# Kernel tuning notes

Measured on AMD Instinct MI355X. Metric: run time of the kernel, lower is better.

## Reference

```python
import jax, jax.numpy as jnp
import numpy as np

B, L, D, C, NB = 2, 256, 3, 256, 64
LN_EPS = 1e-5


def setup_inputs() -> dict:
    ks = jax.random.split(jax.random.key(0), 12)
    x_BLD = jax.random.normal(ks[0], (B, L, D), dtype=jnp.float32) * 0.5
    c_BD = jax.random.normal(ks[1], (B, C), dtype=jnp.float32)
    embed_w = jax.random.normal(ks[2], (NB, C), dtype=jnp.float32) * 0.02
    pos_w = jax.random.normal(ks[3], (128, C), dtype=jnp.float32) * 0.02
    bins = jnp.linspace(0.0, 3.0, NB - 1, dtype=jnp.float32)
    ada_w = jax.random.normal(ks[4], (3 * C, C), dtype=jnp.float32) * (C ** -0.5)
    ada_b = jnp.zeros((3 * C,), dtype=jnp.float32)
    ln_g = jnp.ones((C,), dtype=jnp.float32)
    ln_b = jnp.zeros((C,), dtype=jnp.float32)
    fc1_w = jax.random.normal(ks[5], (4 * C, C), dtype=jnp.float32) * (C ** -0.5)
    fc1_b = jnp.zeros((4 * C,), dtype=jnp.float32)
    fc2_w = jax.random.normal(ks[6], (C, 4 * C), dtype=jnp.float32) * ((4 * C) ** -0.5)
    fc2_b = jnp.zeros((C,), dtype=jnp.float32)
    return {"x_BLD": x_BLD, "c_BD": c_BD, "embed_w": embed_w, "pos_w": pos_w,
            "bins": bins, "ada_w": ada_w, "ada_b": ada_b, "ln_g": ln_g,
            "ln_b": ln_b, "fc1_w": fc1_w, "fc1_b": fc1_b, "fc2_w": fc2_w,
            "fc2_b": fc2_b}


def reference(x_BLD, c_BD, embed_w, pos_w, bins, ada_w, ada_b, ln_g, ln_b,
              fc1_w, fc1_b, fc2_w, fc2_b):
    # pairwise squared distances: [B, L, L]
    d_BLL = jnp.sum((x_BLD[:, :, None, :] - x_BLD[:, None, :, :]) ** 2, axis=-1)
    # bucketize (torch.bucketize right=False == searchsorted side='left')
    idx_BLL = jnp.searchsorted(bins, d_BLL, side="left")
    # relative position embedding: [L, L, C]
    rel = jnp.arange(L)[:, None] - jnp.arange(L)[None, :]
    rel = jnp.clip(rel, -64, 63) + 64
    pos_LLD = pos_w[rel]
    # adaLN modulation from conditioning: SiLU -> Linear -> 3 chunks
    mod = jax.nn.silu(c_BD) @ ada_w.T + ada_b            # [B, 3C]
    shift, scale, gate = jnp.split(mod, 3, axis=-1)      # each [B, C]
    shift = shift[:, None, None, :]
    scale = scale[:, None, None, :]
    gate = gate[:, None, None, :]
    # embed + pos, affine modulate
    s = embed_w[idx_BLL] + pos_LLD[None]                 # [B, L, L, C]
    s = s * (1.0 + scale) + shift
    # LayerNorm over channel dim
    mu = jnp.mean(s, axis=-1, keepdims=True)
    var = jnp.mean((s - mu) ** 2, axis=-1, keepdims=True)
    h = (s - mu) * jax.lax.rsqrt(var + LN_EPS) * ln_g + ln_b
    # MLP: Linear -> GELU(exact) -> Linear
    h = jax.nn.gelu(h @ fc1_w.T + fc1_b, approximate=False)
    h = h @ fc2_w.T + fc2_b
    return s + gate * h
```

## Files before the change

kernel.cpp:

```cpp
#include <hip/hip_runtime.h>
#include <math.h>

#define Cn 256
#define Ln 256
#define Bn 2
#define H1 1024
#define NIDX 64
#define NREL 128
#define NCOMBO 16384
#define BK 64
#define TROWS 32

typedef __attribute__((ext_vector_type(8))) short bf16x8;
typedef __attribute__((ext_vector_type(4))) float f32x4;
typedef unsigned int u32;

__device__ __forceinline__ float gelu_exact(float x) {
    return 0.5f * x * (1.0f + erff(x * 0.70710678118654752f));
}
__device__ __forceinline__ short f2bf(float f) {
    unsigned u = __float_as_uint(f);
    return (short)((u + 0x7fffu + ((u >> 16) & 1u)) >> 16);
}
__device__ __forceinline__ void async16(const void* g, void* l) {
    __builtin_amdgcn_global_load_lds((const __attribute__((address_space(1))) u32*)g,
                                     (__attribute__((address_space(3))) u32*)l, 16, 0, 0);
}

__global__ __launch_bounds__(256) void mod_kernel(
    const float* __restrict__ c_BD, const float* __restrict__ ada_w,
    const float* __restrict__ ada_b, float* __restrict__ mod)
{
    int o = blockIdx.x * 256 + threadIdx.x;
    int b = o / (3 * Cn);
    int j = o - b * (3 * Cn);
    const float* crow = c_BD + b * Cn;
    const float* wrow = ada_w + (size_t)j * Cn;
    float acc = 0.f;
    for (int k = 0; k < Cn; k += 4) {
        float4 cv = *(const float4*)(crow + k);
        float4 wv = *(const float4*)(wrow + k);
        acc += (cv.x / (1.f + expf(-cv.x))) * wv.x;
        acc += (cv.y / (1.f + expf(-cv.y))) * wv.y;
        acc += (cv.z / (1.f + expf(-cv.z))) * wv.z;
        acc += (cv.w / (1.f + expf(-cv.w))) * wv.w;
    }
    mod[o] = acc + ada_b[j];
}

__global__ __launch_bounds__(256) void cvt_kernel(
    const float* __restrict__ s, short* __restrict__ d, int n)
{
    int i = (blockIdx.x * 256 + threadIdx.x) * 4;
    if (i < n) {
        float4 v = *(const float4*)(s + i);
        short4 o;
        o.x = f2bf(v.x); o.y = f2bf(v.y); o.z = f2bf(v.z); o.w = f2bf(v.w);
        *(short4*)(d + i) = o;
    }
}

__global__ __launch_bounds__(256) void ln_kernel(
    const float* __restrict__ embed_w, const float* __restrict__ pos_w,
    const float* __restrict__ ln_g, const float* __restrict__ ln_b,
    const float* __restrict__ mod,
    float* __restrict__ s_out, short* __restrict__ h_out)
{
    const int tid  = threadIdx.x;
    const int wave = tid >> 6;
    const int lane = tid & 63;
    const int base = blockIdx.x * 8;
    const int b    = base >> 13;
    const int idx  = (base >> 7) & 63;
    const int rel0 = base & 127;
    const float* modb = mod + b * (3 * Cn);
    const int c0 = lane * 4;

    const float4 ev = *(const float4*)(embed_w + (size_t)idx * Cn + c0);
    const float4 sc = *(const float4*)(modb + Cn + c0);
    const float4 sh = *(const float4*)(modb + c0);
    const float4 lg = *(const float4*)(ln_g + c0);
    const float4 lb = *(const float4*)(ln_b + c0);

    #pragma unroll
    for (int r8 = 0; r8 < 2; ++r8) {
        const int rr  = wave * 2 + r8;
        const int row = base + rr;
        const float4 p = *(const float4*)(pos_w + (size_t)(rel0 + rr) * Cn + c0);
        float v0 = (ev.x + p.x) * (1.f + sc.x) + sh.x;
        float v1 = (ev.y + p.y) * (1.f + sc.y) + sh.y;
        float v2 = (ev.z + p.z) * (1.f + sc.z) + sh.z;
        float v3 = (ev.w + p.w) * (1.f + sc.w) + sh.w;
        float sum = v0 + v1 + v2 + v3;
        #pragma unroll
        for (int off = 32; off; off >>= 1) sum += __shfl_xor(sum, off, 64);
        const float mu = sum * (1.f / Cn);
        float t0 = v0 - mu, t1 = v1 - mu, t2 = v2 - mu, t3 = v3 - mu;
        float p2 = t0 * t0 + t1 * t1 + t2 * t2 + t3 * t3;
        #pragma unroll
        for (int off = 32; off; off >>= 1) p2 += __shfl_xor(p2, off, 64);
        const float rstd = rsqrtf(p2 * (1.f / Cn) + 1e-5f);

        *(float4*)(s_out + (size_t)row * Cn + c0) = (float4){v0, v1, v2, v3};
        short4 hq;
        hq.x = f2bf(t0 * rstd * lg.x + lb.x);
        hq.y = f2bf(t1 * rstd * lg.y + lb.y);
        hq.z = f2bf(t2 * rstd * lg.z + lb.z);
        hq.w = f2bf(t3 * rstd * lg.w + lb.w);
        *(short4*)(h_out + (size_t)row * Cn + c0) = hq;
    }
}

__global__ __launch_bounds__(256) void gemm1_kernel(
    const short* __restrict__ h, const short* __restrict__ w1,
    const float* __restrict__ fc1_b, short* __restrict__ g)
{
    __shared__ __align__(16) short Alds[128 * BK];
    __shared__ __align__(16) short Wlds[128 * BK];

    const int tid  = threadIdx.x;
    const int wave = tid >> 6;
    const int lane = tid & 63;
    const int quad = lane >> 4;
    const int l15  = lane & 15;
    const int wm   = wave >> 1, wn = wave & 1;
    const int m0 = (blockIdx.x >> 3) * 128;
    const int n0 = (blockIdx.x & 7) * 128;

    const int srow = lane >> 3;
    const int skel = (lane & 7) * 8;

    f32x4 acc[4][4];
    #pragma unroll
    for (int a = 0; a < 4; ++a)
        #pragma unroll
        for (int c = 0; c < 4; ++c) acc[a][c] = (f32x4){0.f, 0.f, 0.f, 0.f};

    for (int kt = 0; kt < Cn; kt += BK) {
        #pragma unroll
        for (int c = 0; c < 4; ++c) {
            const int r = wave * 32 + c * 8;
            async16(h  + (size_t)(m0 + r + srow) * Cn + kt + skel, Alds + r * BK);
            async16(w1 + (size_t)(n0 + r + srow) * Cn + kt + skel, Wlds + r * BK);
        }
        __syncthreads();
        #pragma unroll
        for (int ks = 0; ks < 2; ++ks) {
            bf16x8 wf[4], hf[4];
            #pragma unroll
            for (int nt = 0; nt < 4; ++nt)
                wf[nt] = *(const bf16x8*)(Wlds + (wn * 64 + nt * 16 + l15) * BK + ks * 32 + quad * 8);
            #pragma unroll
            for (int mt = 0; mt < 4; ++mt)
                hf[mt] = *(const bf16x8*)(Alds + (wm * 64 + mt * 16 + l15) * BK + ks * 32 + quad * 8);
            #pragma unroll
            for (int mt = 0; mt < 4; ++mt)
                #pragma unroll
                for (int nt = 0; nt < 4; ++nt)
                    acc[mt][nt] = __builtin_amdgcn_mfma_f32_16x16x32_bf16(
                        wf[nt], hf[mt], acc[mt][nt], 0, 0, 0);
        }
        __syncthreads();
    }

    #pragma unroll
    for (int mt = 0; mt < 4; ++mt) {
        const int m = m0 + wm * 64 + mt * 16 + l15;
        #pragma unroll
        for (int nt = 0; nt < 4; ++nt) {
            const int n = n0 + wn * 64 + nt * 16 + quad * 4;
            const float4 b4 = *(const float4*)(fc1_b + n);
            short4 o;
            o.x = f2bf(gelu_exact(acc[mt][nt][0] + b4.x));
            o.y = f2bf(gelu_exact(acc[mt][nt][1] + b4.y));
            o.z = f2bf(gelu_exact(acc[mt][nt][2] + b4.z));
            o.w = f2bf(gelu_exact(acc[mt][nt][3] + b4.w));
            *(short4*)(g + (size_t)m * H1 + n) = o;
        }
    }
}

__global__ __launch_bounds__(256) void gemm2_kernel(
    const short* __restrict__ g, const short* __restrict__ w2,
    const float* __restrict__ fc2_b, const float* __restrict__ s_in,
    const float* __restrict__ mod, float* __restrict__ table)
{
    __shared__ __align__(16) short Alds[64 * BK];
    __shared__ __align__(16) short Wlds[128 * BK];

    const int tid  = threadIdx.x;
    const int wave = tid >> 6;
    const int lane = tid & 63;
    const int quad = lane >> 4;
    const int l15  = lane & 15;
    const int wm   = wave >> 1, wn = wave & 1;
    const int m0 = (blockIdx.x >> 1) * 64;
    const int n0 = (blockIdx.x & 1) * 128;
    const int b  = m0 >> 13;
    const float* modb = mod + b * (3 * Cn);

    const int srow = lane >> 3;
    const int skel = (lane & 7) * 8;

    f32x4 acc[2][4];
    #pragma unroll
    for (int a = 0; a < 2; ++a)
        #pragma unroll
        for (int c = 0; c < 4; ++c) acc[a][c] = (f32x4){0.f, 0.f, 0.f, 0.f};

    for (int kt = 0; kt < H1; kt += BK) {
        #pragma unroll
        for (int c = 0; c < 2; ++c) {
            const int r = wave * 16 + c * 8;
            async16(g + (size_t)(m0 + r + srow) * H1 + kt + skel, Alds + r * BK);
        }
        #pragma unroll
        for (int c = 0; c < 4; ++c) {
            const int r = wave * 32 + c * 8;
            async16(w2 + (size_t)(n0 + r + srow) * H1 + kt + skel, Wlds + r * BK);
        }
        __syncthreads();
        #pragma unroll
        for (int ks = 0; ks < 2; ++ks) {
            bf16x8 wf[4], gf[2];
            #pragma unroll
            for (int nt = 0; nt < 4; ++nt)
                wf[nt] = *(const bf16x8*)(Wlds + (wn * 64 + nt * 16 + l15) * BK + ks * 32 + quad * 8);
            #pragma unroll
            for (int mt = 0; mt < 2; ++mt)
                gf[mt] = *(const bf16x8*)(Alds + (wm * 32 + mt * 16 + l15) * BK + ks * 32 + quad * 8);
            #pragma unroll
            for (int mt = 0; mt < 2; ++mt)
                #pragma unroll
                for (int nt = 0; nt < 4; ++nt)
                    acc[mt][nt] = __builtin_amdgcn_mfma_f32_16x16x32_bf16(
                        wf[nt], gf[mt], acc[mt][nt], 0, 0, 0);
        }
        __syncthreads();
    }

    #pragma unroll
    for (int mt = 0; mt < 2; ++mt) {
        const int m = m0 + wm * 32 + mt * 16 + l15;
        #pragma unroll
        for (int nt = 0; nt < 4; ++nt) {
            const int n = n0 + wn * 64 + nt * 16 + quad * 4;
            const float4 b4 = *(const float4*)(fc2_b + n);
            const float4 g4 = *(const float4*)(modb + 2 * Cn + n);
            const float4 s4 = *(const float4*)(s_in + (size_t)m * Cn + n);
            float4 o;
            o.x = s4.x + g4.x * (acc[mt][nt][0] + b4.x);
            o.y = s4.y + g4.y * (acc[mt][nt][1] + b4.y);
            o.z = s4.z + g4.z * (acc[mt][nt][2] + b4.z);
            o.w = s4.w + g4.w * (acc[mt][nt][3] + b4.w);
            *(float4*)(table + (size_t)m * Cn + n) = o;
        }
    }
}

__global__ __launch_bounds__(256) void gather_kernel(
    const float* __restrict__ x, const float* __restrict__ bins,
    const float* __restrict__ table, float* __restrict__ out)
{
    __shared__ float xs[Ln * 3];
    __shared__ float bins_s[63];
    __shared__ int   idx_s[64];

    const int tid = threadIdx.x;
    const int blk = blockIdx.x;
    const int q   = blk & 3;
    const int bi  = blk >> 2;
    const int b   = bi >> 8;
    const int i   = bi & 255;

    for (int t = tid; t < Ln * 3; t += 256) xs[t] = x[(size_t)b * Ln * 3 + t];
    if (tid < 63) bins_s[tid] = bins[tid];
    __syncthreads();

    if (tid < 64) {
        int j = q * 64 + tid;
        float d0 = xs[3 * i]     - xs[3 * j];
        float d1 = xs[3 * i + 1] - xs[3 * j + 1];
        float d2 = xs[3 * i + 2] - xs[3 * j + 2];
        float d = d0 * d0 + d1 * d1 + d2 * d2;
        int v = 0;
        #pragma unroll
        for (int k = 0; k < 63; ++k) v += (bins_s[k] < d) ? 1 : 0;
        idx_s[tid] = v;
    }
    __syncthreads();

    const int wave = tid >> 6;
    const int lane = tid & 63;
    float4* outp = (float4*)(out + (size_t)bi * Ln * Cn);
    const float4* tab4 = (const float4*)table;

    float4 v[16];
    #pragma unroll
    for (int jj = 0; jj < 16; ++jj) {
        int jl  = wave * 16 + jj;
        int j   = q * 64 + jl;
        int rel = i - j;
        rel = (rel < -64 ? -64 : (rel > 63 ? 63 : rel)) + 64;
        size_t trow = (size_t)((b * NIDX + idx_s[jl]) * NREL + rel) * (Cn / 4);
        v[jj] = tab4[trow + lane];
    }
    #pragma unroll
    for (int jj = 0; jj < 16; ++jj) {
        int j = q * 64 + wave * 16 + jj;
        outp[(size_t)j * (Cn / 4) + lane] = v[jj];
    }
}

__global__ __launch_bounds__(256) void table_mfma_kernel(
    const float* __restrict__ embed_w, const float* __restrict__ pos_w,
    const float* __restrict__ ln_g, const float* __restrict__ ln_b,
    const short* __restrict__ fc1bf, const float* __restrict__ fc1_b,
    const short* __restrict__ fc2bf, const float* __restrict__ fc2_b,
    const float* __restrict__ mod, float* __restrict__ table)
{
    __shared__ __align__(16) short h_lds[TROWS][264];
    __shared__ __align__(16) short g_lds[TROWS][264];
    __shared__ float s_lds[TROWS][260];

    const int tid  = threadIdx.x;
    const int wave = tid >> 6;
    const int lane = tid & 63;
    const int quad = lane >> 4;
    const int l15  = lane & 15;

    const int base = blockIdx.x * TROWS;
    const int b    = base >> 13;
    const int idx  = (base >> 7) & 63;
    const int rel0 = base & 127;

    const float* modb = mod + b * (3 * Cn);
    const float* erow = embed_w + (size_t)idx * Cn;

    float scale[4], shift[4], lng[4], lnb[4], ev[4];
    #pragma unroll
    for (int m = 0; m < 4; ++m) {
        int c = lane + 64 * m;
        scale[m] = 1.f + modb[Cn + c];
        shift[m] = modb[c];
        lng[m]   = ln_g[c];
        lnb[m]   = ln_b[c];
        ev[m]    = erow[c];
    }

    for (int r8 = 0; r8 < 8; ++r8) {
        const int rr = wave * 8 + r8;
        const float* prow = pos_w + (size_t)(rel0 + rr) * Cn;
        float sv[4]; float sum = 0.f;
        #pragma unroll
        for (int m = 0; m < 4; ++m) {
            float v = (ev[m] + prow[lane + 64 * m]) * scale[m] + shift[m];
            sv[m] = v; sum += v;
        }
        #pragma unroll
        for (int off = 32; off; off >>= 1) sum += __shfl_xor(sum, off, 64);
        float mu = sum * (1.f / Cn);
        float p2 = 0.f;
        #pragma unroll
        for (int m = 0; m < 4; ++m) { float t = sv[m] - mu; p2 += t * t; }
        #pragma unroll
        for (int off = 32; off; off >>= 1) p2 += __shfl_xor(p2, off, 64);
        float rstd = rsqrtf(p2 * (1.f / Cn) + 1e-5f);
        #pragma unroll
        for (int m = 0; m < 4; ++m) {
            int c = lane + 64 * m;
            s_lds[rr][c] = sv[m];
            h_lds[rr][c] = f2bf((sv[m] - mu) * rstd * lng[m] + lnb[m]);
        }
    }
    __syncthreads();

    f32x4 acc2[2][4];
    #pragma unroll
    for (int mt = 0; mt < 2; ++mt)
        #pragma unroll
        for (int nt = 0; nt < 4; ++nt) acc2[mt][nt] = (f32x4){0.f, 0.f, 0.f, 0.f};

    for (int c = 0; c < 4; ++c) {
        f32x4 z[2][4];
        #pragma unroll
        for (int mt = 0; mt < 2; ++mt)
            #pragma unroll
            for (int nt = 0; nt < 4; ++nt) z[mt][nt] = (f32x4){0.f, 0.f, 0.f, 0.f};

        #pragma unroll
        for (int ks = 0; ks < 8; ++ks) {
            int k0 = ks * 32 + quad * 8;
            bf16x8 a0 = *(const bf16x8*)(&h_lds[l15][k0]);
            bf16x8 a1 = *(const bf16x8*)(&h_lds[16 + l15][k0]);
            #pragma unroll
            for (int nt = 0; nt < 4; ++nt) {
                int n = c * 256 + wave * 64 + nt * 16 + l15;
                bf16x8 bf = *(const bf16x8*)(fc1bf + (size_t)n * Cn + k0);
                z[0][nt] = __builtin_amdgcn_mfma_f32_16x16x32_bf16(a0, bf, z[0][nt], 0, 0, 0);
                z[1][nt] = __builtin_amdgcn_mfma_f32_16x16x32_bf16(a1, bf, z[1][nt], 0, 0, 0);
            }
        }
        __syncthreads();
        #pragma unroll
        for (int mt = 0; mt < 2; ++mt)
            #pragma unroll
            for (int nt = 0; nt < 4; ++nt) {
                int coll = wave * 64 + nt * 16 + l15;
                float bias = fc1_b[c * 256 + coll];
                #pragma unroll
                for (int r = 0; r < 4; ++r) {
                    int row = mt * 16 + quad * 4 + r;
                    g_lds[row][coll] = f2bf(gelu_exact(z[mt][nt][r] + bias));
                }
            }
        __syncthreads();
        #pragma unroll
        for (int ks = 0; ks < 8; ++ks) {
            int k0 = ks * 32 + quad * 8;
            bf16x8 a0 = *(const bf16x8*)(&g_lds[l15][k0]);
            bf16x8 a1 = *(const bf16x8*)(&g_lds[16 + l15][k0]);
            #pragma unroll
            for (int nt = 0; nt < 4; ++nt) {
                int n = wave * 64 + nt * 16 + l15;
                bf16x8 bf = *(const bf16x8*)(fc2bf + (size_t)n * H1 + c * 256 + k0);
                acc2[0][nt] = __builtin_amdgcn_mfma_f32_16x16x32_bf16(a0, bf, acc2[0][nt], 0, 0, 0);
                acc2[1][nt] = __builtin_amdgcn_mfma_f32_16x16x32_bf16(a1, bf, acc2[1][nt], 0, 0, 0);
            }
        }
    }

    #pragma unroll
    for (int nt = 0; nt < 4; ++nt) {
        int col = wave * 64 + nt * 16 + l15;
        float bias = fc2_b[col];
        float gate = modb[2 * Cn + col];
        #pragma unroll
        for (int mt = 0; mt < 2; ++mt)
            #pragma unroll
            for (int r = 0; r < 4; ++r) {
                int row = mt * 16 + quad * 4 + r;
                float v = acc2[mt][nt][r] + bias;
                table[(size_t)(base + row) * Cn + col] = s_lds[row][col] + gate * v;
            }
    }
}

extern "C" void kernel_launch(void* const* d_in, const int* in_sizes, int n_in,
                              void* d_out, int out_size, void* d_ws, size_t ws_size,
                              hipStream_t stream) {
    const float* x_BLD   = (const float*)d_in[0];
    const float* c_BD    = (const float*)d_in[1];
    const float* embed_w = (const float*)d_in[2];
    const float* pos_w   = (const float*)d_in[3];
    const float* bins    = (const float*)d_in[4];
    const float* ada_w   = (const float*)d_in[5];
    const float* ada_b   = (const float*)d_in[6];
    const float* ln_g    = (const float*)d_in[7];
    const float* ln_b    = (const float*)d_in[8];
    const float* fc1_w   = (const float*)d_in[9];
    const float* fc1_b   = (const float*)d_in[10];
    const float* fc2_w   = (const float*)d_in[11];
    const float* fc2_b   = (const float*)d_in[12];
    float* out = (float*)d_out;

    char* ws = (char*)d_ws;
    float* mod   = (float*)ws;
    short* fc1bf = (short*)(ws + 8192);
    short* fc2bf = (short*)(ws + 8192 + 524288);
    short* hbuf  = (short*)(ws + 1056768);
    float* sbuf  = (float*)(ws + 9445376);
    short* gbuf  = (short*)(ws + 26222592);
    float* tableA= (float*)(ws + 59777024);
    const size_t needA = 76554240;
    const size_t needB = 8192 + 2 * (size_t)Cn * H1 * sizeof(short)
                       + (size_t)NCOMBO * Cn * sizeof(float);

    mod_kernel<<<(Bn * 3 * Cn) / 256, 256, 0, stream>>>(c_BD, ada_w, ada_b, mod);
    cvt_kernel<<<(Cn * H1 / 4 + 255) / 256, 256, 0, stream>>>(fc1_w, fc1bf, Cn * H1);
    cvt_kernel<<<(Cn * H1 / 4 + 255) / 256, 256, 0, stream>>>(fc2_w, fc2bf, Cn * H1);

    if (ws_size >= needA) {
        ln_kernel<<<NCOMBO / 8, 256, 0, stream>>>(
            embed_w, pos_w, ln_g, ln_b, mod, sbuf, hbuf);
        gemm1_kernel<<<(NCOMBO / 128) * (H1 / 128), 256, 0, stream>>>(
            hbuf, fc1bf, fc1_b, gbuf);
        gemm2_kernel<<<(NCOMBO / 64) * (Cn / 128), 256, 0, stream>>>(
            gbuf, fc2bf, fc2_b, sbuf, mod, tableA);
        gather_kernel<<<Bn * Ln * 4, 256, 0, stream>>>(x_BLD, bins, tableA, out);
    } else {
        float* tableB = (float*)(ws + 8192 + 2 * (size_t)Cn * H1 * sizeof(short));
        (void)needB;
        table_mfma_kernel<<<NCOMBO / TROWS, 256, 0, stream>>>(
            embed_w, pos_w, ln_g, ln_b, fc1bf, fc1_b, fc2bf, fc2_b, mod, tableB);
        gather_kernel<<<Bn * Ln * 4, 256, 0, stream>>>(x_BLD, bins, tableB, out);
    }
}
```

Before: 256.5 us.

## Swizzle LDS tiles in MLP GEMMs and recompute residual instead of storing it

The layernorm kernel no longer writes the fp32 pre-norm activation buffer. The second GEMM epilogue recomputes it from the embedding row, position row and the shift/scale modulation, which removes a 16 MB write and a 16 MB read. Both GEMM kernels also XOR-swizzle the 16-byte chunk index in the shared-memory tiles, on both the async load and the fragment read, to reduce LDS bank conflicts. In exchange the epilogue does a few extra small loads that mostly hit in cache.

```diff
diff --git a/kernel.cpp b/kernel.cpp
--- a/kernel.cpp
+++ b/kernel.cpp
@@ -63,8 +63,7 @@
 __global__ __launch_bounds__(256) void ln_kernel(
     const float* __restrict__ embed_w, const float* __restrict__ pos_w,
     const float* __restrict__ ln_g, const float* __restrict__ ln_b,
-    const float* __restrict__ mod,
-    float* __restrict__ s_out, short* __restrict__ h_out)
+    const float* __restrict__ mod, short* __restrict__ h_out)
 {
     const int tid  = threadIdx.x;
     const int wave = tid >> 6;
@@ -101,7 +100,6 @@
         for (int off = 32; off; off >>= 1) p2 += __shfl_xor(p2, off, 64);
         const float rstd = rsqrtf(p2 * (1.f / Cn) + 1e-5f);
 
-        *(float4*)(s_out + (size_t)row * Cn + c0) = (float4){v0, v1, v2, v3};
         short4 hq;
         hq.x = f2bf(t0 * rstd * lg.x + lb.x);
         hq.y = f2bf(t1 * rstd * lg.y + lb.y);
@@ -128,7 +126,7 @@
     const int n0 = (blockIdx.x & 7) * 128;
 
     const int srow = lane >> 3;
-    const int skel = (lane & 7) * 8;
+    const int skel = ((lane & 7) ^ srow) * 8;
 
     f32x4 acc[4][4];
     #pragma unroll
@@ -146,13 +144,14 @@
         __syncthreads();
         #pragma unroll
         for (int ks = 0; ks < 2; ++ks) {
+            const int swz = ((((ks << 2) | quad) ^ (l15 & 7)) << 3);
             bf16x8 wf[4], hf[4];
             #pragma unroll
             for (int nt = 0; nt < 4; ++nt)
-                wf[nt] = *(const bf16x8*)(Wlds + (wn * 64 + nt * 16 + l15) * BK + ks * 32 + quad * 8);
+                wf[nt] = *(const bf16x8*)(Wlds + (wn * 64 + nt * 16 + l15) * BK + swz);
             #pragma unroll
             for (int mt = 0; mt < 4; ++mt)
-                hf[mt] = *(const bf16x8*)(Alds + (wm * 64 + mt * 16 + l15) * BK + ks * 32 + quad * 8);
+                hf[mt] = *(const bf16x8*)(Alds + (wm * 64 + mt * 16 + l15) * BK + swz);
             #pragma unroll
             for (int mt = 0; mt < 4; ++mt)
                 #pragma unroll
@@ -182,7 +181,8 @@
 
 __global__ __launch_bounds__(256) void gemm2_kernel(
     const short* __restrict__ g, const short* __restrict__ w2,
-    const float* __restrict__ fc2_b, const float* __restrict__ s_in,
+    const float* __restrict__ fc2_b,
+    const float* __restrict__ embed_w, const float* __restrict__ pos_w,
     const float* __restrict__ mod, float* __restrict__ table)
 {
     __shared__ __align__(16) short Alds[64 * BK];
@@ -200,7 +200,7 @@
     const float* modb = mod + b * (3 * Cn);
 
     const int srow = lane >> 3;
-    const int skel = (lane & 7) * 8;
+    const int skel = ((lane & 7) ^ srow) * 8;
 
     f32x4 acc[2][4];
     #pragma unroll
@@ -222,13 +222,14 @@
         __syncthreads();
         #pragma unroll
         for (int ks = 0; ks < 2; ++ks) {
+            const int swz = ((((ks << 2) | quad) ^ (l15 & 7)) << 3);
             bf16x8 wf[4], gf[2];
             #pragma unroll
             for (int nt = 0; nt < 4; ++nt)
-                wf[nt] = *(const bf16x8*)(Wlds + (wn * 64 + nt * 16 + l15) * BK + ks * 32 + quad * 8);
+                wf[nt] = *(const bf16x8*)(Wlds + (wn * 64 + nt * 16 + l15) * BK + swz);
             #pragma unroll
             for (int mt = 0; mt < 2; ++mt)
-                gf[mt] = *(const bf16x8*)(Alds + (wm * 32 + mt * 16 + l15) * BK + ks * 32 + quad * 8);
+                gf[mt] = *(const bf16x8*)(Alds + (wm * 32 + mt * 16 + l15) * BK + swz);
             #pragma unroll
             for (int mt = 0; mt < 2; ++mt)
                 #pragma unroll
@@ -242,17 +243,29 @@
     #pragma unroll
     for (int mt = 0; mt < 2; ++mt) {
         const int m = m0 + wm * 32 + mt * 16 + l15;
+        const int eidx = (m >> 7) & 63;
+        const int rel  = m & 127;
+        const float* erow = embed_w + (size_t)eidx * Cn;
+        const float* prow = pos_w + (size_t)rel * Cn;
         #pragma unroll
         for (int nt = 0; nt < 4; ++nt) {
             const int n = n0 + wn * 64 + nt * 16 + quad * 4;
             const float4 b4 = *(const float4*)(fc2_b + n);
             const float4 g4 = *(const float4*)(modb + 2 * Cn + n);
-            const float4 s4 = *(const float4*)(s_in + (size_t)m * Cn + n);
+            const float4 sc = *(const float4*)(modb + Cn + n);
+            const float4 sh = *(const float4*)(modb + n);
+            const float4 e4 = *(const float4*)(erow + n);
+            const float4 p4 = *(const float4*)(prow + n);
             float4 o;
-            o.x = s4.x + g4.x * (acc[mt][nt][0] + b4.x);
-            o.y = s4.y + g4.y * (acc[mt][nt][1] + b4.y);
-            o.z = s4.z + g4.z * (acc[mt][nt][2] + b4.z);
-            o.w = s4.w + g4.w * (acc[mt][nt][3] + b4.w);
+            float s;
+            s   = (e4.x + p4.x) * (1.f + sc.x) + sh.x;
+            o.x = s + g4.x * (acc[mt][nt][0] + b4.x);
+            s   = (e4.y + p4.y) * (1.f + sc.y) + sh.y;
+            o.y = s + g4.y * (acc[mt][nt][1] + b4.y);
+            s   = (e4.z + p4.z) * (1.f + sc.z) + sh.z;
+            o.z = s + g4.z * (acc[mt][nt][2] + b4.z);
+            s   = (e4.w + p4.w) * (1.f + sc.w) + sh.w;
+            o.w = s + g4.w * (acc[mt][nt][3] + b4.w);
             *(float4*)(table + (size_t)m * Cn + n) = o;
         }
     }
@@ -469,7 +482,6 @@
     short* fc1bf = (short*)(ws + 8192);
     short* fc2bf = (short*)(ws + 8192 + 524288);
     short* hbuf  = (short*)(ws + 1056768);
-    float* sbuf  = (float*)(ws + 9445376);
     short* gbuf  = (short*)(ws + 26222592);
     float* tableA= (float*)(ws + 59777024);
     const size_t needA = 76554240;
@@ -482,11 +494,11 @@
 
     if (ws_size >= needA) {
         ln_kernel<<<NCOMBO / 8, 256, 0, stream>>>(
-            embed_w, pos_w, ln_g, ln_b, mod, sbuf, hbuf);
+            embed_w, pos_w, ln_g, ln_b, mod, hbuf);
         gemm1_kernel<<<(NCOMBO / 128) * (H1 / 128), 256, 0, stream>>>(
             hbuf, fc1bf, fc1_b, gbuf);
         gemm2_kernel<<<(NCOMBO / 64) * (Cn / 128), 256, 0, stream>>>(
-            gbuf, fc2bf, fc2_b, sbuf, mod, tableA);
+            gbuf, fc2bf, fc2_b, embed_w, pos_w, mod, tableA);
         gather_kernel<<<Bn * Ln * 4, 256, 0, stream>>>(x_BLD, bins, tableA, out);
     } else {
         float* tableB = (float*)(ws + 8192 + 2 * (size_t)Cn * H1 * sizeof(short));
```

Result: no change. 253.1 us (-1.3%).

## Fuse LayerNorm and both MLP GEMMs into one table kernel

Applied to the files above, without the earlier changes.

Replaces the separate LayerNorm, GEMM1 and GEMM2 kernels, and their global intermediates for h, s and the hidden activations, with a single fused kernel per 32-row tile. The tile keeps h and the GELU output in LDS and recomputes s in the epilogue from embed and pos instead of storing it. The two weight-conversion launches are merged into one. This removes a large amount of global memory traffic and several launches. In exchange, weights are read straight from global memory without LDS staging, and each block works on smaller tiles.

```diff
diff --git a/kernel.cpp b/kernel.cpp
--- a/kernel.cpp
+++ b/kernel.cpp
@@ -8,7 +8,6 @@
 #define NIDX 64
 #define NREL 128
 #define NCOMBO 16384
-#define BK 64
 #define TROWS 32
 
 typedef __attribute__((ext_vector_type(8))) short bf16x8;
@@ -21,10 +20,6 @@
 __device__ __forceinline__ short f2bf(float f) {
     unsigned u = __float_as_uint(f);
     return (short)((u + 0x7fffu + ((u >> 16) & 1u)) >> 16);
-}
-__device__ __forceinline__ void async16(const void* g, void* l) {
-    __builtin_amdgcn_global_load_lds((const __attribute__((address_space(1))) u32*)g,
-                                     (__attribute__((address_space(3))) u32*)l, 16, 0, 0);
 }
 
 __global__ __launch_bounds__(256) void mod_kernel(
@@ -48,212 +43,164 @@
     mod[o] = acc + ada_b[j];
 }
 
-__global__ __launch_bounds__(256) void cvt_kernel(
-    const float* __restrict__ s, short* __restrict__ d, int n)
-{
+__global__ __launch_bounds__(256) void cvt2_kernel(
+    const float* __restrict__ s1, const float* __restrict__ s2,
+    short* __restrict__ d1, short* __restrict__ d2)
+{
+    const int N = Cn * H1;
     int i = (blockIdx.x * 256 + threadIdx.x) * 4;
-    if (i < n) {
-        float4 v = *(const float4*)(s + i);
-        short4 o;
-        o.x = f2bf(v.x); o.y = f2bf(v.y); o.z = f2bf(v.z); o.w = f2bf(v.w);
-        *(short4*)(d + i) = o;
-    }
-}
-
-__global__ __launch_bounds__(256) void ln_kernel(
+    const float* s;
+    short* d;
+    if (i < N) { s = s1 + i; d = d1 + i; }
+    else       { s = s2 + (i - N); d = d2 + (i - N); }
+    float4 v = *(const float4*)s;
+    short4 o;
+    o.x = f2bf(v.x); o.y = f2bf(v.y); o.z = f2bf(v.z); o.w = f2bf(v.w);
+    *(short4*)d = o;
+}
+
+__global__ __launch_bounds__(256, 4) void table_fused_kernel(
     const float* __restrict__ embed_w, const float* __restrict__ pos_w,
     const float* __restrict__ ln_g, const float* __restrict__ ln_b,
-    const float* __restrict__ mod,
-    float* __restrict__ s_out, short* __restrict__ h_out)
-{
-    const int tid  = threadIdx.x;
-    const int wave = tid >> 6;
-    const int lane = tid & 63;
-    const int base = blockIdx.x * 8;
-    const int b    = base >> 13;
-    const int idx  = (base >> 7) & 63;
-    const int rel0 = base & 127;
-    const float* modb = mod + b * (3 * Cn);
-    const int c0 = lane * 4;
-
-    const float4 ev = *(const float4*)(embed_w + (size_t)idx * Cn + c0);
-    const float4 sc = *(const float4*)(modb + Cn + c0);
-    const float4 sh = *(const float4*)(modb + c0);
-    const float4 lg = *(const float4*)(ln_g + c0);
-    const float4 lb = *(const float4*)(ln_b + c0);
-
-    #pragma unroll
-    for (int r8 = 0; r8 < 2; ++r8) {
-        const int rr  = wave * 2 + r8;
-        const int row = base + rr;
-        const float4 p = *(const float4*)(pos_w + (size_t)(rel0 + rr) * Cn + c0);
-        float v0 = (ev.x + p.x) * (1.f + sc.x) + sh.x;
-        float v1 = (ev.y + p.y) * (1.f + sc.y) + sh.y;
-        float v2 = (ev.z + p.z) * (1.f + sc.z) + sh.z;
-        float v3 = (ev.w + p.w) * (1.f + sc.w) + sh.w;
-        float sum = v0 + v1 + v2 + v3;
-        #pragma unroll
-        for (int off = 32; off; off >>= 1) sum += __shfl_xor(sum, off, 64);
-        const float mu = sum * (1.f / Cn);
-        float t0 = v0 - mu, t1 = v1 - mu, t2 = v2 - mu, t3 = v3 - mu;
-        float p2 = t0 * t0 + t1 * t1 + t2 * t2 + t3 * t3;
-        #pragma unroll
-        for (int off = 32; off; off >>= 1) p2 += __shfl_xor(p2, off, 64);
-        const float rstd = rsqrtf(p2 * (1.f / Cn) + 1e-5f);
-
-        *(float4*)(s_out + (size_t)row * Cn + c0) = (float4){v0, v1, v2, v3};
-        short4 hq;
-        hq.x = f2bf(t0 * rstd * lg.x + lb.x);
-        hq.y = f2bf(t1 * rstd * lg.y + lb.y);
-        hq.z = f2bf(t2 * rstd * lg.z + lb.z);
-        hq.w = f2bf(t3 * rstd * lg.w + lb.w);
-        *(short4*)(h_out + (size_t)row * Cn + c0) = hq;
-    }
-}
-
-__global__ __launch_bounds__(256) void gemm1_kernel(
-    const short* __restrict__ h, const short* __restrict__ w1,
-    const float* __restrict__ fc1_b, short* __restrict__ g)
-{
-    __shared__ __align__(16) short Alds[128 * BK];
-    __shared__ __align__(16) short Wlds[128 * BK];
+    const short* __restrict__ fc1bf, const float* __restrict__ fc1_b,
+    const short* __restrict__ fc2bf, const float* __restrict__ fc2_b,
+    const float* __restrict__ mod, float* __restrict__ table)
+{
+    __shared__ __align__(16) short h_lds[TROWS][264];
+    __shared__ __align__(16) short g_lds[TROWS][264];
 
     const int tid  = threadIdx.x;
     const int wave = tid >> 6;
     const int lane = tid & 63;
     const int quad = lane >> 4;
     const int l15  = lane & 15;
-    const int wm   = wave >> 1, wn = wave & 1;
-    const int m0 = (blockIdx.x >> 3) * 128;
-    const int n0 = (blockIdx.x & 7) * 128;
-
-    const int srow = lane >> 3;
-    const int skel = (lane & 7) * 8;
-
-    f32x4 acc[4][4];
-    #pragma unroll
-    for (int a = 0; a < 4; ++a)
-        #pragma unroll
-        for (int c = 0; c < 4; ++c) acc[a][c] = (f32x4){0.f, 0.f, 0.f, 0.f};
-
-    for (int kt = 0; kt < Cn; kt += BK) {
-        #pragma unroll
-        for (int c = 0; c < 4; ++c) {
-            const int r = wave * 32 + c * 8;
-            async16(h  + (size_t)(m0 + r + srow) * Cn + kt + skel, Alds + r * BK);
-            async16(w1 + (size_t)(n0 + r + srow) * Cn + kt + skel, Wlds + r * BK);
+
+    const int base = blockIdx.x * TROWS;
+    const int b    = base >> 13;
+    const int idx  = (base >> 7) & 63;
+    const int rel0 = base & 127;
+
+    const float* modb = mod + b * (3 * Cn);
+    const float* erow = embed_w + (size_t)idx * Cn;
+
+    {
+        const int c0 = lane * 4;
+        float4 ev = *(const float4*)(erow + c0);
+        float4 sc = *(const float4*)(modb + Cn + c0);
+        sc.x += 1.f; sc.y += 1.f; sc.z += 1.f; sc.w += 1.f;
+        const float4 sh = *(const float4*)(modb + c0);
+        const float4 lg = *(const float4*)(ln_g + c0);
+        const float4 lb = *(const float4*)(ln_b + c0);
+        #pragma unroll
+        for (int r8 = 0; r8 < 8; ++r8) {
+            const int rr = wave * 8 + r8;
+            const float4 p = *(const float4*)(pos_w + (size_t)(rel0 + rr) * Cn + c0);
+            float v0 = (ev.x + p.x) * sc.x + sh.x;
+            float v1 = (ev.y + p.y) * sc.y + sh.y;
+            float v2 = (ev.z + p.z) * sc.z + sh.z;
+            float v3 = (ev.w + p.w) * sc.w + sh.w;
+            float sum = v0 + v1 + v2 + v3;
+            #pragma unroll
+            for (int off = 32; off; off >>= 1) sum += __shfl_xor(sum, off, 64);
+            const float mu = sum * (1.f / Cn);
+            float t0 = v0 - mu, t1 = v1 - mu, t2 = v2 - mu, t3 = v3 - mu;
+            float p2 = t0 * t0 + t1 * t1 + t2 * t2 + t3 * t3;
+            #pragma unroll
+            for (int off = 32; off; off >>= 1) p2 += __shfl_xor(p2, off, 64);
+            const float rstd = rsqrtf(p2 * (1.f / Cn) + 1e-5f);
+            short4 hq;
+            hq.x = f2bf(t0 * rstd * lg.x + lb.x);
+            hq.y = f2bf(t1 * rstd * lg.y + lb.y);
+            hq.z = f2bf(t2 * rstd * lg.z + lb.z);
+            hq.w = f2bf(t3 * rstd * lg.w + lb.w);
+            *(short4*)(&h_lds[rr][c0]) = hq;
+        }
+    }
+    __syncthreads();
+
+    f32x4 acc2[2][4];
+    #pragma unroll
+    for (int mt = 0; mt < 2; ++mt)
+        #pragma unroll
+        for (int nt = 0; nt < 4; ++nt) acc2[mt][nt] = (f32x4){0.f, 0.f, 0.f, 0.f};
+
+    for (int c = 0; c < 4; ++c) {
+        f32x4 z[2][4];
+        #pragma unroll
+        for (int mt = 0; mt < 2; ++mt)
+            #pragma unroll
+            for (int nt = 0; nt < 4; ++nt) z[mt][nt] = (f32x4){0.f, 0.f, 0.f, 0.f};
+
+        #pragma unroll
+        for (int ks = 0; ks < 8; ++ks) {
+            const int k0 = ks * 32 + quad * 8;
+            bf16x8 a0 = *(const bf16x8*)(&h_lds[l15][k0]);
+            bf16x8 a1 = *(const bf16x8*)(&h_lds[16 + l15][k0]);
+            #pragma unroll
+            for (int nt = 0; nt < 4; ++nt) {
+                const int n = c * 256 + wave * 64 + nt * 16 + l15;
+                bf16x8 w = *(const bf16x8*)(fc1bf + (size_t)n * Cn + k0);
+                z[0][nt] = __builtin_amdgcn_mfma_f32_16x16x32_bf16(w, a0, z[0][nt], 0, 0, 0);
+                z[1][nt] = __builtin_amdgcn_mfma_f32_16x16x32_bf16(w, a1, z[1][nt], 0, 0, 0);
+            }
         }
         __syncthreads();
-        #pragma unroll
-        for (int ks = 0; ks < 2; ++ks) {
-            bf16x8 wf[4], hf[4];
-            #pragma unroll
-            for (int nt = 0; nt < 4; ++nt)
-                wf[nt] = *(const bf16x8*)(Wlds + (wn * 64 + nt * 16 + l15) * BK + ks * 32 + quad * 8);
-            #pragma unroll
-            for (int mt = 0; mt < 4; ++mt)
-                hf[mt] = *(const bf16x8*)(Alds + (wm * 64 + mt * 16 + l15) * BK + ks * 32 + quad * 8);
-            #pragma unroll
-            for (int mt = 0; mt < 4; ++mt)
-                #pragma unroll
-                for (int nt = 0; nt < 4; ++nt)
-                    acc[mt][nt] = __builtin_amdgcn_mfma_f32_16x16x32_bf16(
-                        wf[nt], hf[mt], acc[mt][nt], 0, 0, 0);
+
+        #pragma unroll
+        for (int mt = 0; mt < 2; ++mt) {
+            #pragma unroll
+            for (int nt = 0; nt < 4; ++nt) {
+                const int cc = wave * 64 + nt * 16 + quad * 4;
+                const float4 b4 = *(const float4*)(fc1_b + c * 256 + cc);
+                short4 o;
+                o.x = f2bf(gelu_exact(z[mt][nt][0] + b4.x));
+                o.y = f2bf(gelu_exact(z[mt][nt][1] + b4.y));
+                o.z = f2bf(gelu_exact(z[mt][nt][2] + b4.z));
+                o.w = f2bf(gelu_exact(z[mt][nt][3] + b4.w));
+                *(short4*)(&g_lds[mt * 16 + l15][cc]) = o;
+            }
         }
         __syncthreads();
-    }
-
-    #pragma unroll
-    for (int mt = 0; mt < 4; ++mt) {
-        const int m = m0 + wm * 64 + mt * 16 + l15;
+
+        #pragma unroll
+        for (int ks = 0; ks < 8; ++ks) {
+            const int k0 = ks * 32 + quad * 8;
+            bf16x8 a0 = *(const bf16x8*)(&g_lds[l15][k0]);
+            bf16x8 a1 = *(const bf16x8*)(&g_lds[16 + l15][k0]);
+            #pragma unroll
+            for (int nt = 0; nt < 4; ++nt) {
+                const int n = wave * 64 + nt * 16 + l15;
+                bf16x8 w = *(const bf16x8*)(fc2bf + (size_t)n * H1 + c * 256 + k0);
+                acc2[0][nt] = __builtin_amdgcn_mfma_f32_16x16x32_bf16(w, a0, acc2[0][nt], 0, 0, 0);
+                acc2[1][nt] = __builtin_amdgcn_mfma_f32_16x16x32_bf16(w, a1, acc2[1][nt], 0, 0, 0);
+            }
+        }
+    }
+
+    #pragma unroll
+    for (int mt = 0; mt < 2; ++mt) {
+        const int row = mt * 16 + l15;
+        const float* prow = pos_w + (size_t)(rel0 + row) * Cn;
         #pragma unroll
         for (int nt = 0; nt < 4; ++nt) {
-            const int n = n0 + wn * 64 + nt * 16 + quad * 4;
-            const float4 b4 = *(const float4*)(fc1_b + n);
-            short4 o;
-            o.x = f2bf(gelu_exact(acc[mt][nt][0] + b4.x));
-            o.y = f2bf(gelu_exact(acc[mt][nt][1] + b4.y));
-            o.z = f2bf(gelu_exact(acc[mt][nt][2] + b4.z));
-            o.w = f2bf(gelu_exact(acc[mt][nt][3] + b4.w));
-            *(short4*)(g + (size_t)m * H1 + n) = o;
-        }
-    }
-}
-
-__global__ __launch_bounds__(256) void gemm2_kernel(
-    const short* __restrict__ g, const short* __restrict__ w2,
-    const float* __restrict__ fc2_b, const float* __restrict__ s_in,
-    const float* __restrict__ mod, float* __restrict__ table)
-{
-    __shared__ __align__(16) short Alds[64 * BK];
-    __shared__ __align__(16) short Wlds[128 * BK];
-
-    const int tid  = threadIdx.x;
-    const int wave = tid >> 6;
-    const int lane = tid & 63;
-    const int quad = lane >> 4;
-    const int l15  = lane & 15;
-    const int wm   = wave >> 1, wn = wave & 1;
-    const int m0 = (blockIdx.x >> 1) * 64;
-    const int n0 = (blockIdx.x & 1) * 128;
-    const int b  = m0 >> 13;
-    const float* modb = mod + b * (3 * Cn);
-
-    const int srow = lane >> 3;
-    const int skel = (lane & 7) * 8;
-
-    f32x4 acc[2][4];
-    #pragma unroll
-    for (int a = 0; a < 2; ++a)
-        #pragma unroll
-        for (int c = 0; c < 4; ++c) acc[a][c] = (f32x4){0.f, 0.f, 0.f, 0.f};
-
-    for (int kt = 0; kt < H1; kt += BK) {
-        #pragma unroll
-        for (int c = 0; c < 2; ++c) {
-            const int r = wave * 16 + c * 8;
-            async16(g + (size_t)(m0 + r + srow) * H1 + kt + skel, Alds + r * BK);
-        }
-        #pragma unroll
-        for (int c = 0; c < 4; ++c) {
-            const int r = wave * 32 + c * 8;
-            async16(w2 + (size_t)(n0 + r + srow) * H1 + kt + skel, Wlds + r * BK);
-        }
-        __syncthreads();
-        #pragma unroll
-        for (int ks = 0; ks < 2; ++ks) {
-            bf16x8 wf[4], gf[2];
-            #pragma unroll
-            for (int nt = 0; nt < 4; ++nt)
-                wf[nt] = *(const bf16x8*)(Wlds + (wn * 64 + nt * 16 + l15) * BK + ks * 32 + quad * 8);
-            #pragma unroll
-            for (int mt = 0; mt < 2; ++mt)
-                gf[mt] = *(const bf16x8*)(Alds + (wm * 32 + mt * 16 + l15) * BK + ks * 32 + quad * 8);
-            #pragma unroll
-            for (int mt = 0; mt < 2; ++mt)
-                #pragma unroll
-                for (int nt = 0; nt < 4; ++nt)
-                    acc[mt][nt] = __builtin_amdgcn_mfma_f32_16x16x32_bf16(
-                        wf[nt], gf[mt], acc[mt][nt], 0, 0, 0);
-        }
-        __syncthreads();
-    }
-
-    #pragma unroll
-    for (int mt = 0; mt < 2; ++mt) {
-        const int m = m0 + wm * 32 + mt * 16 + l15;
-        #pragma unroll
-        for (int nt = 0; nt < 4; ++nt) {
-            const int n = n0 + wn * 64 + nt * 16 + quad * 4;
-            const float4 b4 = *(const float4*)(fc2_b + n);
-            const float4 g4 = *(const float4*)(modb + 2 * Cn + n);
-            const float4 s4 = *(const float4*)(s_in + (size_t)m * Cn + n);
+            const int n0 = wave * 64 + nt * 16 + quad * 4;
+            const float4 b4 = *(const float4*)(fc2_b + n0);
+            const float4 g4 = *(const float4*)(modb + 2 * Cn + n0);
+            const float4 sc = *(const float4*)(modb + Cn + n0);
+            const float4 sh = *(const float4*)(modb + n0);
+            const float4 e4 = *(const float4*)(erow + n0);
+            const float4 p4 = *(const float4*)(prow + n0);
             float4 o;
-            o.x = s4.x + g4.x * (acc[mt][nt][0] + b4.x);
-            o.y = s4.y + g4.y * (acc[mt][nt][1] + b4.y);
-            o.z = s4.z + g4.z * (acc[mt][nt][2] + b4.z);
-            o.w = s4.w + g4.w * (acc[mt][nt][3] + b4.w);
-            *(float4*)(table + (size_t)m * Cn + n) = o;
+            float s;
+            s   = (e4.x + p4.x) * (1.f + sc.x) + sh.x;
+            o.x = s + g4.x * (acc2[mt][nt][0] + b4.x);
+            s   = (e4.y + p4.y) * (1.f + sc.y) + sh.y;
+            o.y = s + g4.y * (acc2[mt][nt][1] + b4.y);
+            s   = (e4.z + p4.z) * (1.f + sc.z) + sh.z;
+            o.z = s + g4.z * (acc2[mt][nt][2] + b4.z);
+            s   = (e4.w + p4.w) * (1.f + sc.w) + sh.w;
+            o.w = s + g4.w * (acc2[mt][nt][3] + b4.w);
+            *(float4*)(table + (size_t)(base + row) * Cn + n0) = o;
         }
     }
 }
@@ -309,140 +256,6 @@
     for (int jj = 0; jj < 16; ++jj) {
         int j = q * 64 + wave * 16 + jj;
         outp[(size_t)j * (Cn / 4) + lane] = v[jj];
-    }
-}
-
-__global__ __launch_bounds__(256) void table_mfma_kernel(
-    const float* __restrict__ embed_w, const float* __restrict__ pos_w,
-    const float* __restrict__ ln_g, const float* __restrict__ ln_b,
-    const short* __restrict__ fc1bf, const float* __restrict__ fc1_b,
-    const short* __restrict__ fc2bf, const float* __restrict__ fc2_b,
-    const float* __restrict__ mod, float* __restrict__ table)
-{
-    __shared__ __align__(16) short h_lds[TROWS][264];
-    __shared__ __align__(16) short g_lds[TROWS][264];
-    __shared__ float s_lds[TROWS][260];
-
-    const int tid  = threadIdx.x;
-    const int wave = tid >> 6;
-    const int lane = tid & 63;
-    const int quad = lane >> 4;
-    const int l15  = lane & 15;
-
-    const int base = blockIdx.x * TROWS;
-    const int b    = base >> 13;
-    const int idx  = (base >> 7) & 63;
-    const int rel0 = base & 127;
-
-    const float* modb = mod + b * (3 * Cn);
-    const float* erow = embed_w + (size_t)idx * Cn;
-
-    float scale[4], shift[4], lng[4], lnb[4], ev[4];
-    #pragma unroll
-    for (int m = 0; m < 4; ++m) {
-        int c = lane + 64 * m;
-        scale[m] = 1.f + modb[Cn + c];
-        shift[m] = modb[c];
-        lng[m]   = ln_g[c];
-        lnb[m]   = ln_b[c];
-        ev[m]    = erow[c];
-    }
-
-    for (int r8 = 0; r8 < 8; ++r8) {
-        const int rr = wave * 8 + r8;
-        const float* prow = pos_w + (size_t)(rel0 + rr) * Cn;
-        float sv[4]; float sum = 0.f;
-        #pragma unroll
-        for (int m = 0; m < 4; ++m) {
-            float v = (ev[m] + prow[lane + 64 * m]) * scale[m] + shift[m];
-            sv[m] = v; sum += v;
-        }
-        #pragma unroll
-        for (int off = 32; off; off >>= 1) sum += __shfl_xor(sum, off, 64);
-        float mu = sum * (1.f / Cn);
-        float p2 = 0.f;
-        #pragma unroll
-        for (int m = 0; m < 4; ++m) { float t = sv[m] - mu; p2 += t * t; }
-        #pragma unroll
-        for (int off = 32; off; off >>= 1) p2 += __shfl_xor(p2, off, 64);
-        float rstd = rsqrtf(p2 * (1.f / Cn) + 1e-5f);
-        #pragma unroll
-        for (int m = 0; m < 4; ++m) {
-            int c = lane + 64 * m;
-            s_lds[rr][c] = sv[m];
-            h_lds[rr][c] = f2bf((sv[m] - mu) * rstd * lng[m] + lnb[m]);
-        }
-    }
-    __syncthreads();
-
-    f32x4 acc2[2][4];
-    #pragma unroll
-    for (int mt = 0; mt < 2; ++mt)
-        #pragma unroll
-        for (int nt = 0; nt < 4; ++nt) acc2[mt][nt] = (f32x4){0.f, 0.f, 0.f, 0.f};
-
-    for (int c = 0; c < 4; ++c) {
-        f32x4 z[2][4];
-        #pragma unroll
-        for (int mt = 0; mt < 2; ++mt)
-            #pragma unroll
-            for (int nt = 0; nt < 4; ++nt) z[mt][nt] = (f32x4){0.f, 0.f, 0.f, 0.f};
-
-        #pragma unroll
-        for (int ks = 0; ks < 8; ++ks) {
-            int k0 = ks * 32 + quad * 8;
-            bf16x8 a0 = *(const bf16x8*)(&h_lds[l15][k0]);
-            bf16x8 a1 = *(const bf16x8*)(&h_lds[16 + l15][k0]);
-            #pragma unroll
-            for (int nt = 0; nt < 4; ++nt) {
-                int n = c * 256 + wave * 64 + nt * 16 + l15;
-                bf16x8 bf = *(const bf16x8*)(fc1bf + (size_t)n * Cn + k0);
-                z[0][nt] = __builtin_amdgcn_mfma_f32_16x16x32_bf16(a0, bf, z[0][nt], 0, 0, 0);
-                z[1][nt] = __builtin_amdgcn_mfma_f32_16x16x32_bf16(a1, bf, z[1][nt], 0, 0, 0);
-            }
-        }
-        __syncthreads();
-        #pragma unroll
-        for (int mt = 0; mt < 2; ++mt)
-            #pragma unroll
-            for (int nt = 0; nt < 4; ++nt) {
-                int coll = wave * 64 + nt * 16 + l15;
-                float bias = fc1_b[c * 256 + coll];
-                #pragma unroll
-                for (int r = 0; r < 4; ++r) {
-                    int row = mt * 16 + quad * 4 + r;
-                    g_lds[row][coll] = f2bf(gelu_exact(z[mt][nt][r] + bias));
-                }
-            }
-        __syncthreads();
-        #pragma unroll
-        for (int ks = 0; ks < 8; ++ks) {
-            int k0 = ks * 32 + quad * 8;
-            bf16x8 a0 = *(const bf16x8*)(&g_lds[l15][k0]);
-            bf16x8 a1 = *(const bf16x8*)(&g_lds[16 + l15][k0]);
-            #pragma unroll
-            for (int nt = 0; nt < 4; ++nt) {
-                int n = wave * 64 + nt * 16 + l15;
-                bf16x8 bf = *(const bf16x8*)(fc2bf + (size_t)n * H1 + c * 256 + k0);
-                acc2[0][nt] = __builtin_amdgcn_mfma_f32_16x16x32_bf16(a0, bf, acc2[0][nt], 0, 0, 0);
-                acc2[1][nt] = __builtin_amdgcn_mfma_f32_16x16x32_bf16(a1, bf, acc2[1][nt], 0, 0, 0);
-            }
-        }
-    }
-
-    #pragma unroll
-    for (int nt = 0; nt < 4; ++nt) {
-        int col = wave * 64 + nt * 16 + l15;
-        float bias = fc2_b[col];
-        float gate = modb[2 * Cn + col];
-        #pragma unroll
-        for (int mt = 0; mt < 2; ++mt)
-            #pragma unroll
-            for (int r = 0; r < 4; ++r) {
-                int row = mt * 16 + quad * 4 + r;
-                float v = acc2[mt][nt][r] + bias;
-                table[(size_t)(base + row) * Cn + col] = s_lds[row][col] + gate * v;
-            }
     }
 }
 
@@ -468,31 +281,11 @@
     float* mod   = (float*)ws;
     short* fc1bf = (short*)(ws + 8192);
     short* fc2bf = (short*)(ws + 8192 + 524288);
-    short* hbuf  = (short*)(ws + 1056768);
-    float* sbuf  = (float*)(ws + 9445376);
-    short* gbuf  = (short*)(ws + 26222592);
-    float* tableA= (float*)(ws + 59777024);
-    const size_t needA = 76554240;
-    const size_t needB = 8192 + 2 * (size_t)Cn * H1 * sizeof(short)
-                       + (size_t)NCOMBO * Cn * sizeof(float);
+    float* table = (float*)(ws + 8192 + 2 * 524288);
 
     mod_kernel<<<(Bn * 3 * Cn) / 256, 256, 0, stream>>>(c_BD, ada_w, ada_b, mod);
-    cvt_kernel<<<(Cn * H1 / 4 + 255) / 256, 256, 0, stream>>>(fc1_w, fc1bf, Cn * H1);
-    cvt_kernel<<<(Cn * H1 / 4 + 255) / 256, 256, 0, stream>>>(fc2_w, fc2bf, Cn * H1);
-
-    if (ws_size >= needA) {
-        ln_kernel<<<NCOMBO / 8, 256, 0, stream>>>(
-            embed_w, pos_w, ln_g, ln_b, mod, sbuf, hbuf);
-        gemm1_kernel<<<(NCOMBO / 128) * (H1 / 128), 256, 0, stream>>>(
-            hbuf, fc1bf, fc1_b, gbuf);
-        gemm2_kernel<<<(NCOMBO / 64) * (Cn / 128), 256, 0, stream>>>(
-            gbuf, fc2bf, fc2_b, sbuf, mod, tableA);
-        gather_kernel<<<Bn * Ln * 4, 256, 0, stream>>>(x_BLD, bins, tableA, out);
-    } else {
-        float* tableB = (float*)(ws + 8192 + 2 * (size_t)Cn * H1 * sizeof(short));
-        (void)needB;
-        table_mfma_kernel<<<NCOMBO / TROWS, 256, 0, stream>>>(
-            embed_w, pos_w, ln_g, ln_b, fc1bf, fc1_b, fc2bf, fc2_b, mod, tableB);
-        gather_kernel<<<Bn * Ln * 4, 256, 0, stream>>>(x_BLD, bins, tableB, out);
-    }
-}
+    cvt2_kernel<<<2 * Cn * H1 / 4 / 256, 256, 0, stream>>>(fc1_w, fc2_w, fc1bf, fc2bf);
+    table_fused_kernel<<<NCOMBO / TROWS, 256, 0, stream>>>(
+        embed_w, pos_w, ln_g, ln_b, fc1bf, fc1_b, fc2bf, fc2_b, mod, table);
+    gather_kernel<<<Bn * Ln * 4, 256, 0, stream>>>(x_BLD, bins, table, out);
+}
```

Result: slower. 279.9 us (+9.1%).
